# Optimization experiments

Measured on AMD Instinct MI355X. Metric: run time of the kernel, lower is better.

The kernel has to match this reference:

```python
import jax, jax.numpy as jnp
import numpy as np

B, HS, WS = 4, 64, 64
UP = 8
H, W = HS * UP, WS * UP
C_ORI, C_MNT, C_OFF = 90, 180, 8
K = 1024            # max minutiae candidates per image (64*64 cells max 4096)
THRESH = 0.5
DIST_T = 16.0
ANG_T = np.pi / 6


def setup_inputs() -> dict:
    key = jax.random.key(0)
    ks = jax.random.split(key, 8)
    return {
        'segmentation': jax.random.uniform(ks[0], (B, 1, HS, WS), jnp.float32),
        'segmentation_up': jax.random.uniform(ks[1], (B, 1, H, W), jnp.float32),
        'orientation_up': jax.random.normal(ks[2], (B, C_ORI, H, W), jnp.float32),
        'enhanced_real': jax.random.normal(ks[3], (B, 1, H, W), jnp.float32),
        'minutiae_score': jax.random.uniform(ks[4], (B, 1, HS, WS), jnp.float32),
        'minutiae_orientation': jax.random.normal(ks[5], (B, C_MNT, HS, WS), jnp.float32),
        'minutiae_x_offset': jax.random.normal(ks[6], (B, C_OFF, HS, WS), jnp.float32),
        'minutiae_y_offset': jax.random.normal(ks[7], (B, C_OFF, HS, WS), jnp.float32),
    }


def _opening(x, k):
    # morphological opening (erosion then dilation) with a k x k ones kernel,
    # separable min/max pooling; geodesic border (pad so border is neutral).
    pl, pr = (k - 1) // 2, k // 2

    def pool(v, comp, init, pad_val):
        vp = jnp.pad(v, ((0, 0), (pl, pr), (pl, pr)), constant_values=pad_val)
        vp = jax.lax.reduce_window(vp, init, comp, (1, k, 1), (1, 1, 1), 'VALID')
        return jax.lax.reduce_window(vp, init, comp, (1, 1, k), (1, 1, 1), 'VALID')

    er = pool(x, jax.lax.min, np.inf, 1e4)
    return pool(er, jax.lax.max, -np.inf, -1e4)


def _nms_keep(xy, ang, valid):
    # xy: [K,2], ang: [K], valid: [K] bool; entries already sorted by score desc
    d = jnp.sqrt(jnp.sum((xy[:, None, :] - xy[None, :, :]) ** 2, axis=-1))
    da = jnp.abs(ang[:, None] - ang[None, :])
    da = jnp.minimum(da, 2 * jnp.pi - da)
    sup = (d < DIST_T) & (da < ANG_T) & valid[:, None] & valid[None, :]
    idxs = jnp.arange(K)

    def body(i, keep):
        return keep & ~(sup[i] & (idxs > i) & keep[i])

    return jax.lax.fori_loop(0, K, body, valid)


def _detect(score, ori, xo, yo):
    # score: [HS,WS]; ori: [C_MNT,HS,WS]; xo/yo: [C_OFF,HS,WS]
    h, w = score.shape
    flat = score.reshape(-1)
    masked = jnp.where(flat > THRESH, flat, -1.0)
    vals, idx = jax.lax.top_k(masked, K)          # sorted descending
    valid = vals > THRESH
    rows = idx // w
    cols = idx % w
    ang_idx = jnp.argmax(ori.reshape(C_MNT, -1)[:, idx], axis=0)
    xoff = jnp.argmax(xo.reshape(C_OFF, -1)[:, idx], axis=0)
    yoff = jnp.argmax(yo.reshape(C_OFF, -1)[:, idx], axis=0)
    angles = (ang_idx.astype(jnp.float32) * 2.0 - 89.0) * (np.pi / 180.0)
    xc = cols.astype(jnp.float32) * 8.0 + xoff.astype(jnp.float32)
    yc = rows.astype(jnp.float32) * 8.0 + yoff.astype(jnp.float32)
    scores = flat[idx]
    m = jnp.stack([xc, yc, angles, scores], axis=-1)  # [K,4]
    keep = _nms_keep(m[:, :2], angles, valid)
    return m, keep


def reference(segmentation, segmentation_up, orientation_up, enhanced_real,
              minutiae_score, minutiae_orientation, minutiae_x_offset,
              minutiae_y_offset):
    mask = _opening(jnp.round(segmentation[:, 0]), 5)          # [B,HS,WS]
    mask_up = _opening(jnp.round(segmentation_up[:, 0]), 5 * UP)  # [B,H,W]

    score = minutiae_score[:, 0] * mask
    minut, keep = jax.vmap(_detect)(score, minutiae_orientation,
                                    minutiae_x_offset, minutiae_y_offset)
    minut = minut * keep[..., None].astype(minut.dtype)       # zero suppressed

    ori_field = (jnp.argmax(orientation_up, axis=1).astype(jnp.float32) * 2.0
                 - 90.0) * (np.pi / 180.0) * mask_up

    enh = enhanced_real[:, 0] * mask_up
    ef = enh.reshape(B, -1)
    emin = ef.min(axis=1, keepdims=True)
    emax = ef.max(axis=1, keepdims=True)
    enh_vis = ((ef - emin) / (emax - emin + 1e-8)).reshape(B, H, W) * 255.0

    return (minut, keep.astype(jnp.float32), enh_vis, mask_up * 255.0, ori_field)
```

## Files before the change

kernel.cpp:

```cpp
#include <hip/hip_runtime.h>
#include <math.h>

#define HSd 64
#define WSd 64
#define Hh 512
#define Wh 512
#define Bn 4
#define C_ORIc 90
#define C_MNTc 180
#define C_OFFc 8
#define Kc 1024

#define O_MINUT 0
#define O_KEEP  (Bn*Kc*4)
#define O_VIS   (O_KEEP + Bn*Kc)
#define O_MASK  (O_VIS + Bn*Hh*Wh)
#define O_ORI   (O_MASK + Bn*Hh*Wh)

#define PI_180 0.017453292519943295f
#define TWO_PI 6.283185307179586f
#define ANG_T  0.5235987755982988f

template <bool ISMIN, bool BIN>
__global__ __launch_bounds__(256) void pass_v(const float* __restrict__ in,
                                              float* __restrict__ out)
{
    int c = blockIdx.x * 64 + threadIdx.x;
    int r = blockIdx.y * 4 + threadIdx.y;
    int b = blockIdx.z;
    const float* p = in + (size_t)b * Hh * Wh;
    int lo = max(r - 19, 0), hi = min(r + 20, Hh - 1);
    float acc = ISMIN ? 1e30f : -1e30f;
    for (int rr = lo; rr <= hi; rr++) {
        float v = p[rr * Wh + c];
        if (BIN) v = rintf(v);
        acc = ISMIN ? fminf(acc, v) : fmaxf(acc, v);
    }
    out[(size_t)b * Hh * Wh + (size_t)r * Wh + c] = acc;
}

template <bool ISMIN>
__global__ __launch_bounds__(256) void pass_h(const float* __restrict__ in,
                                              float* __restrict__ out)
{
    int c = blockIdx.x * 64 + threadIdx.x;
    int r = blockIdx.y * 4 + threadIdx.y;
    int b = blockIdx.z;
    const float* p = in + (size_t)b * Hh * Wh + (size_t)r * Wh;
    int lo = max(c - 19, 0), hi = min(c + 20, Wh - 1);
    float acc = ISMIN ? 1e30f : -1e30f;
    for (int cc = lo; cc <= hi; cc++)
        acc = ISMIN ? fminf(acc, p[cc]) : fmaxf(acc, p[cc]);
    out[(size_t)b * Hh * Wh + (size_t)r * Wh + c] = acc;
}

__global__ __launch_bounds__(512) void final_up_kernel(const float* __restrict__ vmx,
                                                       const float* __restrict__ ori,
                                                       const float* __restrict__ enh,
                                                       float* __restrict__ out,
                                                       float* __restrict__ partials)
{
    int r = blockIdx.x, b = blockIdx.y, c = threadIdx.x;
    __shared__ float row[512];
    __shared__ float rmn[512];
    __shared__ float rmx[512];
    size_t base = (size_t)b * Hh * Wh + (size_t)r * Wh;
    row[c] = vmx[base + c];
    __syncthreads();
    int lo = max(c - 19, 0), hi = min(c + 20, Wh - 1);
    float m = -1e30f;
    for (int cc = lo; cc <= hi; cc++) m = fmaxf(m, row[cc]);
    out[O_MASK + base + c] = m * 255.0f;

    float of = 0.0f;
    if (m != 0.0f) {
        const float* op = ori + (size_t)b * C_ORIc * Hh * Wh + (size_t)r * Wh + c;
        float best = op[0];
        int bi = 0;
        for (int ch = 1; ch < C_ORIc; ch++) {
            float v = op[(size_t)ch * Hh * Wh];
            if (v > best) { best = v; bi = ch; }
        }
        of = ((float)bi * 2.0f - 90.0f) * PI_180 * m;
    }
    out[O_ORI + base + c] = of;

    float e = enh[base + c] * m;
    rmn[c] = e; rmx[c] = e;
    __syncthreads();
    for (int s2 = 256; s2 > 0; s2 >>= 1) {
        if (c < s2) {
            rmn[c] = fminf(rmn[c], rmn[c + s2]);
            rmx[c] = fmaxf(rmx[c], rmx[c + s2]);
        }
        __syncthreads();
    }
    if (c == 0) {
        partials[(b * Hh + r) * 2 + 0] = rmn[0];
        partials[(b * Hh + r) * 2 + 1] = rmx[0];
    }
}

__global__ __launch_bounds__(512) void reduce_mm_kernel(const float* __restrict__ partials,
                                                        float* __restrict__ mm)
{
    int b = blockIdx.x, t = threadIdx.x;
    __shared__ float mn[512];
    __shared__ float mx[512];
    mn[t] = partials[(b * 512 + t) * 2 + 0];
    mx[t] = partials[(b * 512 + t) * 2 + 1];
    __syncthreads();
    for (int s = 256; s > 0; s >>= 1) {
        if (t < s) {
            mn[t] = fminf(mn[t], mn[t + s]);
            mx[t] = fmaxf(mx[t], mx[t + s]);
        }
        __syncthreads();
    }
    if (t == 0) { mm[b * 2] = mn[0]; mm[b * 2 + 1] = mx[0]; }
}

__global__ __launch_bounds__(256) void vis_kernel(const float* __restrict__ enh,
                                                  const float* __restrict__ maskout,
                                                  const float* __restrict__ mm,
                                                  float* __restrict__ vis)
{
    int idx = blockIdx.x * 256 + threadIdx.x;
    int b = idx >> 18;
    float m = (maskout[idx] != 0.0f) ? 1.0f : 0.0f;
    float e = enh[idx] * m;
    float emin = mm[b * 2], emax = mm[b * 2 + 1];
    float r = (e - emin) / (emax - emin + 1e-8f);
    vis[idx] = r * 255.0f;
}

__global__ __launch_bounds__(1024) void detect_kernel(const float* __restrict__ mscore,
                                                      const float* __restrict__ seg,
                                                      const float* __restrict__ mo,
                                                      const float* __restrict__ xo,
                                                      const float* __restrict__ yo,
                                                      float* __restrict__ out)
{
    int b = blockIdx.x;
    int tid = threadIdx.x;
    __shared__ unsigned long long keys[4096];
    __shared__ float maskT[64][65];
    float* scratch = (float*)keys;

    const float* sg = seg + b * 4096;
    for (int i = tid; i < 4096; i += 1024)
        maskT[i >> 6][i & 63] = rintf(sg[i]);
    __syncthreads();
    for (int i = tid; i < 4096; i += 1024) {
        int r = i >> 6, c = i & 63;
        int lo = max(r - 2, 0), hi = min(r + 2, 63);
        float m = 1e30f;
        for (int rr = lo; rr <= hi; rr++) m = fminf(m, maskT[rr][c]);
        scratch[r * 65 + c] = m;
    }
    __syncthreads();
    for (int i = tid; i < 4096; i += 1024) {
        int r = i >> 6, c = i & 63;
        int lo = max(c - 2, 0), hi = min(c + 2, 63);
        float m = 1e30f;
        for (int cc = lo; cc <= hi; cc++) m = fminf(m, scratch[r * 65 + cc]);
        maskT[r][c] = m;
    }
    __syncthreads();
    for (int i = tid; i < 4096; i += 1024) {
        int r = i >> 6, c = i & 63;
        int lo = max(r - 2, 0), hi = min(r + 2, 63);
        float m = -1e30f;
        for (int rr = lo; rr <= hi; rr++) m = fmaxf(m, maskT[rr][c]);
        scratch[r * 65 + c] = m;
    }
    __syncthreads();
    for (int i = tid; i < 4096; i += 1024) {
        int r = i >> 6, c = i & 63;
        int lo = max(c - 2, 0), hi = min(c + 2, 63);
        float m = -1e30f;
        for (int cc = lo; cc <= hi; cc++) m = fmaxf(m, scratch[r * 65 + cc]);
        maskT[r][c] = m;
    }
    __syncthreads();

    const float* sp = mscore + b * 4096;
    bool anyv = false;
    for (int i = tid; i < 4096; i += 1024) {
        float s = sp[i] * maskT[i >> 6][i & 63];
        anyv |= (s > 0.5f);
    }
    if (!__syncthreads_or(anyv)) {
        float* mout = out + O_MINUT + (size_t)b * Kc * 4 + (size_t)tid * 4;
        mout[0] = 0.f; mout[1] = 0.f; mout[2] = 0.f; mout[3] = 0.f;
        out[O_KEEP + b * Kc + tid] = 0.f;
        return;
    }

    for (int i = tid; i < 4096; i += 1024) {
        float s = sp[i] * maskT[i >> 6][i & 63];
        float mval = (s > 0.5f) ? s : -1.0f;
        unsigned int fb = __float_as_uint(mval);
        unsigned int od = (fb & 0x80000000u) ? ~fb : (fb | 0x80000000u);
        keys[i] = ((unsigned long long)(~od) << 32) | (unsigned int)i;
    }
    for (int k = 2; k <= 4096; k <<= 1) {
        for (int j = k >> 1; j > 0; j >>= 1) {
            __syncthreads();
            for (int t = tid; t < 4096; t += 1024) {
                int ixj = t ^ j;
                if (ixj > t) {
                    unsigned long long va = keys[t], vb = keys[ixj];
                    bool up = ((t & k) == 0);
                    if ((va > vb) == up) { keys[t] = vb; keys[ixj] = va; }
                }
            }
        }
    }
    __syncthreads();

    int idx = (int)(keys[tid] & 0xffffffffu);
    float s = sp[idx] * maskT[idx >> 6][idx & 63];
    bool valid = s > 0.5f;
    int Nv = __syncthreads_count(valid);

    float* sx = scratch;
    float* sy = scratch + 1024;
    float* sa = scratch + 2048;
    int*   keep = (int*)(scratch + 3072);

    float xc = 0.f, yc = 0.f, ang = 0.f;
    if (tid < Nv) {
        int rr = idx >> 6, cc = idx & 63;
        const float* op = mo + (size_t)b * C_MNTc * 4096 + idx;
        float best = op[0]; int bi = 0;
        for (int ch = 1; ch < C_MNTc; ch++) {
            float v = op[ch * 4096];
            if (v > best) { best = v; bi = ch; }
        }
        const float* xp = xo + (size_t)b * C_OFFc * 4096 + idx;
        float bxv = xp[0]; int bx = 0;
        for (int ch = 1; ch < C_OFFc; ch++) {
            float v = xp[ch * 4096];
            if (v > bxv) { bxv = v; bx = ch; }
        }
        const float* yp = yo + (size_t)b * C_OFFc * 4096 + idx;
        float byv = yp[0]; int by = 0;
        for (int ch = 1; ch < C_OFFc; ch++) {
            float v = yp[ch * 4096];
            if (v > byv) { byv = v; by = ch; }
        }
        ang = ((float)bi * 2.0f - 89.0f) * PI_180;
        xc = (float)cc * 8.0f + (float)bx;
        yc = (float)rr * 8.0f + (float)by;
        sx[tid] = xc; sy[tid] = yc; sa[tid] = ang;
        keep[tid] = 1;
    } else {
        keep[tid] = 0;
    }
    __syncthreads();

    for (int i = 0; i < Nv; i++) {
        if (keep[i] && tid > i && tid < Nv && keep[tid]) {
            float dx = sx[tid] - sx[i], dy = sy[tid] - sy[i];
            float d = sqrtf(dx * dx + dy * dy);
            float da = fabsf(sa[tid] - sa[i]);
            da = fminf(da, TWO_PI - da);
            if (d < 16.0f && da < ANG_T) keep[tid] = 0;
        }
        __syncthreads();
    }

    int kf = keep[tid];
    float* mout = out + O_MINUT + (size_t)b * Kc * 4 + (size_t)tid * 4;
    if (kf) {
        mout[0] = xc; mout[1] = yc; mout[2] = ang; mout[3] = s;
    } else {
        mout[0] = 0.f; mout[1] = 0.f; mout[2] = 0.f; mout[3] = 0.f;
    }
    out[O_KEEP + b * Kc + tid] = (float)kf;
}

extern "C" void kernel_launch(void* const* d_in, const int* in_sizes, int n_in,
                              void* d_out_, int out_size, void* d_ws, size_t ws_size,
                              hipStream_t stream)
{
    const float* seg    = (const float*)d_in[0];
    const float* segup  = (const float*)d_in[1];
    const float* oriup  = (const float*)d_in[2];
    const float* enh    = (const float*)d_in[3];
    const float* mscore = (const float*)d_in[4];
    const float* mori   = (const float*)d_in[5];
    const float* mxo    = (const float*)d_in[6];
    const float* myo    = (const float*)d_in[7];
    float* out = (float*)d_out_;

    float* partials = (float*)d_ws;
    float* mm       = partials + Bn * 512 * 2;

    float* T1 = out + O_VIS;
    float* T2 = out + O_ORI;

    detect_kernel<<<Bn, 1024, 0, stream>>>(mscore, seg, mori, mxo, myo, out);

    dim3 pb(64, 4);
    dim3 pg(8, 128, Bn);
    pass_v<true, true><<<pg, pb, 0, stream>>>(segup, T1);
    pass_h<true><<<pg, pb, 0, stream>>>(T1, T2);
    pass_v<false, false><<<pg, pb, 0, stream>>>(T2, T1);
    final_up_kernel<<<dim3(Hh, Bn), 512, 0, stream>>>(T1, oriup, enh, out, partials);
    reduce_mm_kernel<<<Bn, 512, 0, stream>>>(partials, mm);
    vis_kernel<<<(Bn * Hh * Wh) / 256, 256, 0, stream>>>(enh, out + O_MASK, mm, out + O_VIS);
}
```

Before: 511.8 us.

## Fuse detect with vertical erosion and register-block morphology passes

Detection now runs inside the first vertical erosion launch as extra blocks, so the two overlap instead of running as a separate serial kernel. The morphology passes give each thread 4 outputs that share a 37-tap core window, cutting redundant loads, and use float4 IO. The separate min/max reduce kernel is replaced by atomicMin/atomicMax on order-preserving encoded floats, and the detect mask becomes a bitmask. Detection now uses 256 threads with 4 slots each, which may lengthen the serial sort and NMS loops.

```diff
diff --git a/kernel.cpp b/kernel.cpp
--- a/kernel.cpp
+++ b/kernel.cpp
@@ -1,8 +1,6 @@
 #include <hip/hip_runtime.h>
 #include <math.h>
 
-#define HSd 64
-#define WSd 64
 #define Hh 512
 #define Wh 512
 #define Bn 4
@@ -21,264 +19,375 @@
 #define TWO_PI 6.283185307179586f
 #define ANG_T  0.5235987755982988f
 
+#define IMG    262144
+#define PB     (256*Bn)
+
+__device__ __forceinline__ unsigned enc_f(float f) {
+    unsigned u = __float_as_uint(f);
+    return (u & 0x80000000u) ? ~u : (u | 0x80000000u);
+}
+__device__ __forceinline__ float dec_f(unsigned e) {
+    return __uint_as_float((e & 0x80000000u) ? (e ^ 0x80000000u) : ~e);
+}
+
 template <bool ISMIN, bool BIN>
-__global__ __launch_bounds__(256) void pass_v(const float* __restrict__ in,
-                                              float* __restrict__ out)
-{
-    int c = blockIdx.x * 64 + threadIdx.x;
-    int r = blockIdx.y * 4 + threadIdx.y;
-    int b = blockIdx.z;
-    const float* p = in + (size_t)b * Hh * Wh;
-    int lo = max(r - 19, 0), hi = min(r + 20, Hh - 1);
-    float acc = ISMIN ? 1e30f : -1e30f;
-    for (int rr = lo; rr <= hi; rr++) {
-        float v = p[rr * Wh + c];
-        if (BIN) v = rintf(v);
-        acc = ISMIN ? fminf(acc, v) : fmaxf(acc, v);
-    }
-    out[(size_t)b * Hh * Wh + (size_t)r * Wh + c] = acc;
-}
-
-template <bool ISMIN>
-__global__ __launch_bounds__(256) void pass_h(const float* __restrict__ in,
-                                              float* __restrict__ out)
-{
-    int c = blockIdx.x * 64 + threadIdx.x;
-    int r = blockIdx.y * 4 + threadIdx.y;
-    int b = blockIdx.z;
-    const float* p = in + (size_t)b * Hh * Wh + (size_t)r * Wh;
-    int lo = max(c - 19, 0), hi = min(c + 20, Wh - 1);
-    float acc = ISMIN ? 1e30f : -1e30f;
-    for (int cc = lo; cc <= hi; cc++)
-        acc = ISMIN ? fminf(acc, p[cc]) : fmaxf(acc, p[cc]);
-    out[(size_t)b * Hh * Wh + (size_t)r * Wh + c] = acc;
-}
-
-__global__ __launch_bounds__(512) void final_up_kernel(const float* __restrict__ vmx,
-                                                       const float* __restrict__ ori,
-                                                       const float* __restrict__ enh,
-                                                       float* __restrict__ out,
-                                                       float* __restrict__ partials)
-{
-    int r = blockIdx.x, b = blockIdx.y, c = threadIdx.x;
-    __shared__ float row[512];
-    __shared__ float rmn[512];
-    __shared__ float rmx[512];
-    size_t base = (size_t)b * Hh * Wh + (size_t)r * Wh;
-    row[c] = vmx[base + c];
-    __syncthreads();
-    int lo = max(c - 19, 0), hi = min(c + 20, Wh - 1);
-    float m = -1e30f;
-    for (int cc = lo; cc <= hi; cc++) m = fmaxf(m, row[cc]);
-    out[O_MASK + base + c] = m * 255.0f;
-
-    float of = 0.0f;
-    if (m != 0.0f) {
-        const float* op = ori + (size_t)b * C_ORIc * Hh * Wh + (size_t)r * Wh + c;
-        float best = op[0];
-        int bi = 0;
-        for (int ch = 1; ch < C_ORIc; ch++) {
-            float v = op[(size_t)ch * Hh * Wh];
-            if (v > best) { best = v; bi = ch; }
-        }
-        of = ((float)bi * 2.0f - 90.0f) * PI_180 * m;
-    }
-    out[O_ORI + base + c] = of;
-
-    float e = enh[base + c] * m;
-    rmn[c] = e; rmx[c] = e;
-    __syncthreads();
-    for (int s2 = 256; s2 > 0; s2 >>= 1) {
-        if (c < s2) {
-            rmn[c] = fminf(rmn[c], rmn[c + s2]);
-            rmx[c] = fmaxf(rmx[c], rmx[c + s2]);
-        }
-        __syncthreads();
-    }
-    if (c == 0) {
-        partials[(b * Hh + r) * 2 + 0] = rmn[0];
-        partials[(b * Hh + r) * 2 + 1] = rmx[0];
-    }
-}
-
-__global__ __launch_bounds__(512) void reduce_mm_kernel(const float* __restrict__ partials,
-                                                        float* __restrict__ mm)
-{
-    int b = blockIdx.x, t = threadIdx.x;
-    __shared__ float mn[512];
-    __shared__ float mx[512];
-    mn[t] = partials[(b * 512 + t) * 2 + 0];
-    mx[t] = partials[(b * 512 + t) * 2 + 1];
-    __syncthreads();
-    for (int s = 256; s > 0; s >>= 1) {
-        if (t < s) {
-            mn[t] = fminf(mn[t], mn[t + s]);
-            mx[t] = fmaxf(mx[t], mx[t + s]);
-        }
-        __syncthreads();
-    }
-    if (t == 0) { mm[b * 2] = mn[0]; mm[b * 2 + 1] = mx[0]; }
-}
-
-__global__ __launch_bounds__(256) void vis_kernel(const float* __restrict__ enh,
-                                                  const float* __restrict__ maskout,
-                                                  const float* __restrict__ mm,
-                                                  float* __restrict__ vis)
-{
-    int idx = blockIdx.x * 256 + threadIdx.x;
-    int b = idx >> 18;
-    float m = (maskout[idx] != 0.0f) ? 1.0f : 0.0f;
-    float e = enh[idx] * m;
-    float emin = mm[b * 2], emax = mm[b * 2 + 1];
-    float r = (e - emin) / (emax - emin + 1e-8f);
-    vis[idx] = r * 255.0f;
-}
-
-__global__ __launch_bounds__(1024) void detect_kernel(const float* __restrict__ mscore,
-                                                      const float* __restrict__ seg,
-                                                      const float* __restrict__ mo,
-                                                      const float* __restrict__ xo,
-                                                      const float* __restrict__ yo,
-                                                      float* __restrict__ out)
-{
-    int b = blockIdx.x;
+__device__ __forceinline__ void vert_pass_body(const float* __restrict__ in,
+                                               float* __restrict__ outp, int blk)
+{
+    const float SENT = ISMIN ? 1e30f : -1e30f;
+    int b  = blk >> 8;
+    int rg = (blk >> 3) & 31;
+    int cg = blk & 7;
+    int tx = threadIdx.x & 63, ty = threadIdx.x >> 6;
+    int c  = cg * 64 + tx;
+    int r0 = rg * 16 + ty * 4;
+    const float* p = in + (size_t)b * IMG + c;
+
+    #define LDV(rr) (((rr) >= 0 && (rr) < 512) ? (BIN ? rintf(p[(rr) * 512]) \
+                                                      : p[(rr) * 512]) : SENT)
+    #define OPV(a, bb) (ISMIN ? fminf(a, bb) : fmaxf(a, bb))
+    float core = SENT;
+    #pragma unroll
+    for (int k = 0; k < 37; k++) core = OPV(core, LDV(r0 - 16 + k));
+    float L2v = LDV(r0 - 17);
+    float L1v = OPV(LDV(r0 - 18), L2v);
+    float L0v = OPV(LDV(r0 - 19), L1v);
+    float H1v = LDV(r0 + 21);
+    float H2v = OPV(H1v, LDV(r0 + 22));
+    float H3v = OPV(H2v, LDV(r0 + 23));
+    float* q = outp + (size_t)b * IMG + (size_t)r0 * 512 + c;
+    q[0]    = OPV(core, L0v);
+    q[512]  = OPV(core, OPV(L1v, H1v));
+    q[1024] = OPV(core, OPV(L2v, H2v));
+    q[1536] = OPV(core, H3v);
+    #undef LDV
+    #undef OPV
+}
+
+__global__ __launch_bounds__(256) void k1_vert_erode_detect(
+    const float* __restrict__ segup, const float* __restrict__ mscore,
+    const float* __restrict__ seg, const float* __restrict__ mo,
+    const float* __restrict__ xo, const float* __restrict__ yo,
+    float* __restrict__ out, float* __restrict__ T1, unsigned* __restrict__ mmu)
+{
+    __shared__ union {
+        unsigned long long keys[4096];
+        float scr[8320];
+    } U;
+    __shared__ unsigned smBits[128];
+    __shared__ unsigned short smHalf[256];
+
     int tid = threadIdx.x;
-    __shared__ unsigned long long keys[4096];
-    __shared__ float maskT[64][65];
-    float* scratch = (float*)keys;
+    if (blockIdx.x < PB) {
+        vert_pass_body<true, true>(segup, T1, blockIdx.x);
+        return;
+    }
+
+    int b = blockIdx.x - PB;
+    if (tid == 0) { mmu[b * 2] = 0xFFFFFFFFu; mmu[b * 2 + 1] = 0u; }
 
     const float* sg = seg + b * 4096;
-    for (int i = tid; i < 4096; i += 1024)
-        maskT[i >> 6][i & 63] = rintf(sg[i]);
-    __syncthreads();
-    for (int i = tid; i < 4096; i += 1024) {
+    float* scr0 = U.scr;
+    float* scr1 = U.scr + 4160;
+    for (int i = tid; i < 4096; i += 256)
+        scr0[(i >> 6) * 65 + (i & 63)] = rintf(sg[i]);
+    __syncthreads();
+    for (int i = tid; i < 4096; i += 256) {
         int r = i >> 6, c = i & 63;
         int lo = max(r - 2, 0), hi = min(r + 2, 63);
         float m = 1e30f;
-        for (int rr = lo; rr <= hi; rr++) m = fminf(m, maskT[rr][c]);
-        scratch[r * 65 + c] = m;
-    }
-    __syncthreads();
-    for (int i = tid; i < 4096; i += 1024) {
+        for (int rr = lo; rr <= hi; rr++) m = fminf(m, scr0[rr * 65 + c]);
+        scr1[r * 65 + c] = m;
+    }
+    __syncthreads();
+    for (int i = tid; i < 4096; i += 256) {
         int r = i >> 6, c = i & 63;
         int lo = max(c - 2, 0), hi = min(c + 2, 63);
         float m = 1e30f;
-        for (int cc = lo; cc <= hi; cc++) m = fminf(m, scratch[r * 65 + cc]);
-        maskT[r][c] = m;
-    }
-    __syncthreads();
-    for (int i = tid; i < 4096; i += 1024) {
+        for (int cc = lo; cc <= hi; cc++) m = fminf(m, scr1[r * 65 + cc]);
+        scr0[r * 65 + c] = m;
+    }
+    __syncthreads();
+    for (int i = tid; i < 4096; i += 256) {
         int r = i >> 6, c = i & 63;
         int lo = max(r - 2, 0), hi = min(r + 2, 63);
         float m = -1e30f;
-        for (int rr = lo; rr <= hi; rr++) m = fmaxf(m, maskT[rr][c]);
-        scratch[r * 65 + c] = m;
-    }
-    __syncthreads();
-    for (int i = tid; i < 4096; i += 1024) {
-        int r = i >> 6, c = i & 63;
-        int lo = max(c - 2, 0), hi = min(c + 2, 63);
-        float m = -1e30f;
-        for (int cc = lo; cc <= hi; cc++) m = fmaxf(m, scratch[r * 65 + cc]);
-        maskT[r][c] = m;
-    }
+        for (int rr = lo; rr <= hi; rr++) m = fmaxf(m, scr0[rr * 65 + c]);
+        scr1[r * 65 + c] = m;
+    }
+    __syncthreads();
+    {
+        unsigned short bits16 = 0;
+        int i0 = tid * 16;
+        int r = i0 >> 6;
+        for (int j = 0; j < 16; j++) {
+            int c = (i0 + j) & 63;
+            int lo = max(c - 2, 0), hi = min(c + 2, 63);
+            float m = -1e30f;
+            for (int cc = lo; cc <= hi; cc++) m = fmaxf(m, scr1[r * 65 + cc]);
+            bits16 |= ((unsigned short)(m != 0.0f)) << j;
+        }
+        smHalf[tid] = bits16;
+    }
+    __syncthreads();
+    if (tid < 128)
+        smBits[tid] = (unsigned)smHalf[2 * tid] | ((unsigned)smHalf[2 * tid + 1] << 16);
     __syncthreads();
 
     const float* sp = mscore + b * 4096;
     bool anyv = false;
-    for (int i = tid; i < 4096; i += 1024) {
-        float s = sp[i] * maskT[i >> 6][i & 63];
-        anyv |= (s > 0.5f);
+    for (int i = tid; i < 4096; i += 256) {
+        unsigned m = (smBits[i >> 5] >> (i & 31)) & 1u;
+        anyv |= (m && sp[i] > 0.5f);
     }
     if (!__syncthreads_or(anyv)) {
-        float* mout = out + O_MINUT + (size_t)b * Kc * 4 + (size_t)tid * 4;
-        mout[0] = 0.f; mout[1] = 0.f; mout[2] = 0.f; mout[3] = 0.f;
-        out[O_KEEP + b * Kc + tid] = 0.f;
+        float4 z = {0.f, 0.f, 0.f, 0.f};
+        float4* mo4 = (float4*)(out + O_MINUT + (size_t)b * 4096);
+        for (int i = tid; i < 1024; i += 256) mo4[i] = z;
+        ((float4*)(out + O_KEEP + (size_t)b * 1024))[tid] = z;
         return;
     }
 
-    for (int i = tid; i < 4096; i += 1024) {
-        float s = sp[i] * maskT[i >> 6][i & 63];
+    for (int i = tid; i < 4096; i += 256) {
+        unsigned m = (smBits[i >> 5] >> (i & 31)) & 1u;
+        float s = m ? sp[i] : 0.0f;
         float mval = (s > 0.5f) ? s : -1.0f;
-        unsigned int fb = __float_as_uint(mval);
-        unsigned int od = (fb & 0x80000000u) ? ~fb : (fb | 0x80000000u);
-        keys[i] = ((unsigned long long)(~od) << 32) | (unsigned int)i;
+        unsigned fb = __float_as_uint(mval);
+        unsigned od = (fb & 0x80000000u) ? ~fb : (fb | 0x80000000u);
+        U.keys[i] = ((unsigned long long)(~od) << 32) | (unsigned)i;
     }
     for (int k = 2; k <= 4096; k <<= 1) {
         for (int j = k >> 1; j > 0; j >>= 1) {
             __syncthreads();
-            for (int t = tid; t < 4096; t += 1024) {
+            for (int t = tid; t < 4096; t += 256) {
                 int ixj = t ^ j;
                 if (ixj > t) {
-                    unsigned long long va = keys[t], vb = keys[ixj];
+                    unsigned long long va = U.keys[t], vb = U.keys[ixj];
                     bool up = ((t & k) == 0);
-                    if ((va > vb) == up) { keys[t] = vb; keys[ixj] = va; }
+                    if ((va > vb) == up) { U.keys[t] = vb; U.keys[ixj] = va; }
                 }
             }
         }
     }
     __syncthreads();
 
-    int idx = (int)(keys[tid] & 0xffffffffu);
-    float s = sp[idx] * maskT[idx >> 6][idx & 63];
-    bool valid = s > 0.5f;
-    int Nv = __syncthreads_count(valid);
-
-    float* sx = scratch;
-    float* sy = scratch + 1024;
-    float* sa = scratch + 2048;
-    int*   keep = (int*)(scratch + 3072);
-
-    float xc = 0.f, yc = 0.f, ang = 0.f;
-    if (tid < Nv) {
-        int rr = idx >> 6, cc = idx & 63;
-        const float* op = mo + (size_t)b * C_MNTc * 4096 + idx;
-        float best = op[0]; int bi = 0;
-        for (int ch = 1; ch < C_MNTc; ch++) {
-            float v = op[ch * 4096];
-            if (v > best) { best = v; bi = ch; }
-        }
-        const float* xp = xo + (size_t)b * C_OFFc * 4096 + idx;
-        float bxv = xp[0]; int bx = 0;
-        for (int ch = 1; ch < C_OFFc; ch++) {
-            float v = xp[ch * 4096];
-            if (v > bxv) { bxv = v; bx = ch; }
-        }
-        const float* yp = yo + (size_t)b * C_OFFc * 4096 + idx;
-        float byv = yp[0]; int by = 0;
-        for (int ch = 1; ch < C_OFFc; ch++) {
-            float v = yp[ch * 4096];
-            if (v > byv) { byv = v; by = ch; }
-        }
-        ang = ((float)bi * 2.0f - 89.0f) * PI_180;
-        xc = (float)cc * 8.0f + (float)bx;
-        yc = (float)rr * 8.0f + (float)by;
-        sx[tid] = xc; sy[tid] = yc; sa[tid] = ang;
-        keep[tid] = 1;
-    } else {
-        keep[tid] = 0;
+    int idxs[4]; float ss[4]; int vld[4];
+    int Nv = 0;
+    for (int j = 0; j < 4; j++) {
+        int slot = tid + j * 256;
+        int idx = (int)(U.keys[slot] & 0xffffffffu);
+        unsigned m = (smBits[idx >> 5] >> (idx & 31)) & 1u;
+        float s = m ? sp[idx] : 0.0f;
+        idxs[j] = idx; ss[j] = s; vld[j] = (s > 0.5f);
+        Nv += __syncthreads_count(vld[j]);
+    }
+
+    float xcs[4], ycs[4], angs[4];
+    for (int j = 0; j < 4; j++) {
+        int slot = tid + j * 256;
+        xcs[j] = ycs[j] = angs[j] = 0.f;
+        if (slot < Nv) {
+            int idx = idxs[j];
+            int rr = idx >> 6, cc = idx & 63;
+            const float* op_ = mo + (size_t)b * C_MNTc * 4096 + idx;
+            float best = op_[0]; int bi = 0;
+            for (int ch = 1; ch < C_MNTc; ch++) {
+                float v = op_[ch * 4096];
+                if (v > best) { best = v; bi = ch; }
+            }
+            const float* xp = xo + (size_t)b * C_OFFc * 4096 + idx;
+            float bxv = xp[0]; int bx = 0;
+            for (int ch = 1; ch < C_OFFc; ch++) {
+                float v = xp[ch * 4096];
+                if (v > bxv) { bxv = v; bx = ch; }
+            }
+            const float* yp = yo + (size_t)b * C_OFFc * 4096 + idx;
+            float byv = yp[0]; int by = 0;
+            for (int ch = 1; ch < C_OFFc; ch++) {
+                float v = yp[ch * 4096];
+                if (v > byv) { byv = v; by = ch; }
+            }
+            angs[j] = ((float)bi * 2.0f - 89.0f) * PI_180;
+            xcs[j]  = (float)cc * 8.0f + (float)bx;
+            ycs[j]  = (float)rr * 8.0f + (float)by;
+        }
+    }
+    __syncthreads();
+    float* sx = U.scr;
+    float* sy = U.scr + 1024;
+    float* sa = U.scr + 2048;
+    int*   keep = (int*)(U.scr + 3072);
+    for (int j = 0; j < 4; j++) {
+        int slot = tid + j * 256;
+        sx[slot] = xcs[j]; sy[slot] = ycs[j]; sa[slot] = angs[j];
+        keep[slot] = (slot < Nv) ? 1 : 0;
     }
     __syncthreads();
 
     for (int i = 0; i < Nv; i++) {
-        if (keep[i] && tid > i && tid < Nv && keep[tid]) {
-            float dx = sx[tid] - sx[i], dy = sy[tid] - sy[i];
-            float d = sqrtf(dx * dx + dy * dy);
-            float da = fabsf(sa[tid] - sa[i]);
-            da = fminf(da, TWO_PI - da);
-            if (d < 16.0f && da < ANG_T) keep[tid] = 0;
+        if (keep[i]) {
+            float xi = sx[i], yi = sy[i], ai = sa[i];
+            for (int j = 0; j < 4; j++) {
+                int slot = tid + j * 256;
+                if (slot > i && slot < Nv && keep[slot]) {
+                    float dx = xcs[j] - xi, dy = ycs[j] - yi;
+                    float d = sqrtf(dx * dx + dy * dy);
+                    float da = fabsf(angs[j] - ai);
+                    da = fminf(da, TWO_PI - da);
+                    if (d < 16.0f && da < ANG_T) keep[slot] = 0;
+                }
+            }
         }
         __syncthreads();
     }
-
-    int kf = keep[tid];
-    float* mout = out + O_MINUT + (size_t)b * Kc * 4 + (size_t)tid * 4;
-    if (kf) {
-        mout[0] = xc; mout[1] = yc; mout[2] = ang; mout[3] = s;
-    } else {
-        mout[0] = 0.f; mout[1] = 0.f; mout[2] = 0.f; mout[3] = 0.f;
-    }
-    out[O_KEEP + b * Kc + tid] = (float)kf;
+    for (int j = 0; j < 4; j++) {
+        int slot = tid + j * 256;
+        int kf = keep[slot];
+        float* mout = out + O_MINUT + (size_t)b * 4096 + slot * 4;
+        if (kf) {
+            mout[0] = xcs[j]; mout[1] = ycs[j]; mout[2] = angs[j]; mout[3] = ss[j];
+        } else {
+            mout[0] = 0.f; mout[1] = 0.f; mout[2] = 0.f; mout[3] = 0.f;
+        }
+        out[O_KEEP + b * 1024 + slot] = (float)kf;
+    }
+}
+
+__global__ __launch_bounds__(512) void k2_horiz_erode(const float* __restrict__ T1,
+                                                      float* __restrict__ T2)
+{
+    __shared__ float row[4][512];
+    int b = blockIdx.y;
+    int r0 = blockIdx.x * 4;
+    int tx = threadIdx.x, ty = threadIdx.y;
+    const float* p = T1 + (size_t)b * IMG + (size_t)(r0 + ty) * 512;
+    ((float4*)row[ty])[tx] = ((const float4*)p)[tx];
+    __syncthreads();
+    int c0 = tx * 4;
+    const float* rw = row[ty];
+    #define LDH(cc) (((cc) >= 0 && (cc) < 512) ? rw[cc] : 1e30f)
+    float core = 1e30f;
+    #pragma unroll
+    for (int k = 0; k < 37; k++) core = fminf(core, LDH(c0 - 16 + k));
+    float L2v = LDH(c0 - 17);
+    float L1v = fminf(LDH(c0 - 18), L2v);
+    float L0v = fminf(LDH(c0 - 19), L1v);
+    float H1v = LDH(c0 + 21);
+    float H2v = fminf(H1v, LDH(c0 + 22));
+    float H3v = fminf(H2v, LDH(c0 + 23));
+    #undef LDH
+    float4 o;
+    o.x = fminf(core, L0v);
+    o.y = fminf(core, fminf(L1v, H1v));
+    o.z = fminf(core, fminf(L2v, H2v));
+    o.w = fminf(core, H3v);
+    ((float4*)(T2 + (size_t)b * IMG + (size_t)(r0 + ty) * 512))[tx] = o;
+}
+
+__global__ __launch_bounds__(256) void k3_vert_dilate(const float* __restrict__ T2,
+                                                      float* __restrict__ T3)
+{
+    vert_pass_body<false, false>(T2, T3, blockIdx.x);
+}
+
+__global__ __launch_bounds__(512) void k4_final(const float* __restrict__ T3,
+                                                const float* __restrict__ ori,
+                                                const float* __restrict__ enh,
+                                                float* __restrict__ out,
+                                                unsigned* __restrict__ mmu)
+{
+    __shared__ float row[4][512];
+    __shared__ float red[512];
+    int b = blockIdx.y;
+    int r0 = blockIdx.x * 4;
+    int tx = threadIdx.x, ty = threadIdx.y;
+    int ltid = ty * 128 + tx;
+    const float* p = T3 + (size_t)b * IMG + (size_t)(r0 + ty) * 512;
+    ((float4*)row[ty])[tx] = ((const float4*)p)[tx];
+    __syncthreads();
+    int c0 = tx * 4;
+    const float* rw = row[ty];
+    #define LDD(cc) (((cc) >= 0 && (cc) < 512) ? rw[cc] : -1e30f)
+    float core = -1e30f;
+    #pragma unroll
+    for (int k = 0; k < 37; k++) core = fmaxf(core, LDD(c0 - 16 + k));
+    float L2v = LDD(c0 - 17);
+    float L1v = fmaxf(LDD(c0 - 18), L2v);
+    float L0v = fmaxf(LDD(c0 - 19), L1v);
+    float H1v = LDD(c0 + 21);
+    float H2v = fmaxf(H1v, LDD(c0 + 22));
+    float H3v = fmaxf(H2v, LDD(c0 + 23));
+    #undef LDD
+    float m[4];
+    m[0] = fmaxf(core, L0v);
+    m[1] = fmaxf(core, fmaxf(L1v, H1v));
+    m[2] = fmaxf(core, fmaxf(L2v, H2v));
+    m[3] = fmaxf(core, H3v);
+
+    size_t base = (size_t)b * IMG + (size_t)(r0 + ty) * 512 + c0;
+    float4 mk = {m[0] * 255.f, m[1] * 255.f, m[2] * 255.f, m[3] * 255.f};
+    *((float4*)(out + O_MASK + base)) = mk;
+
+    float ov[4];
+    for (int j = 0; j < 4; j++) {
+        ov[j] = 0.0f;
+        if (m[j] != 0.0f) {
+            const float* op_ = ori + (size_t)b * C_ORIc * IMG
+                             + (size_t)(r0 + ty) * 512 + (c0 + j);
+            float best = op_[0];
+            int bi = 0;
+            for (int ch = 1; ch < C_ORIc; ch++) {
+                float v = op_[(size_t)ch * IMG];
+                if (v > best) { best = v; bi = ch; }
+            }
+            ov[j] = ((float)bi * 2.0f - 90.0f) * PI_180 * m[j];
+        }
+    }
+    float4 o4 = {ov[0], ov[1], ov[2], ov[3]};
+    *((float4*)(out + O_ORI + base)) = o4;
+
+    float4 e4 = ((const float4*)(enh + (size_t)b * IMG + (size_t)(r0 + ty) * 512))[tx];
+    float e0 = e4.x * m[0], e1 = e4.y * m[1], e2 = e4.z * m[2], e3 = e4.w * m[3];
+    float lmin = fminf(fminf(e0, e1), fminf(e2, e3));
+    float lmax = fmaxf(fmaxf(e0, e1), fmaxf(e2, e3));
+
+    red[ltid] = lmin;
+    __syncthreads();
+    for (int s = 256; s > 0; s >>= 1) {
+        if (ltid < s) red[ltid] = fminf(red[ltid], red[ltid + s]);
+        __syncthreads();
+    }
+    float bmin = red[0];
+    __syncthreads();
+    red[ltid] = lmax;
+    __syncthreads();
+    for (int s = 256; s > 0; s >>= 1) {
+        if (ltid < s) red[ltid] = fmaxf(red[ltid], red[ltid + s]);
+        __syncthreads();
+    }
+    if (ltid == 0) {
+        atomicMin(&mmu[b * 2 + 0], enc_f(bmin));
+        atomicMax(&mmu[b * 2 + 1], enc_f(red[0]));
+    }
+}
+
+__global__ __launch_bounds__(256) void k5_vis(const float* __restrict__ enh,
+                                              const float* __restrict__ maskout,
+                                              const unsigned* __restrict__ mmu,
+                                              float* __restrict__ vis)
+{
+    int i4 = blockIdx.x * 256 + threadIdx.x;
+    int b = i4 >> 16;
+    float4 e = ((const float4*)enh)[i4];
+    float4 mk = ((const float4*)maskout)[i4];
+    float emin = dec_f(mmu[b * 2]);
+    float den = dec_f(mmu[b * 2 + 1]) - emin + 1e-8f;
+    float4 o;
+    o.x = (e.x * (mk.x != 0.f ? 1.f : 0.f) - emin) / den * 255.0f;
+    o.y = (e.y * (mk.y != 0.f ? 1.f : 0.f) - emin) / den * 255.0f;
+    o.z = (e.z * (mk.z != 0.f ? 1.f : 0.f) - emin) / den * 255.0f;
+    o.w = (e.w * (mk.w != 0.f ? 1.f : 0.f) - emin) / den * 255.0f;
+    ((float4*)vis)[i4] = o;
 }
 
 extern "C" void kernel_launch(void* const* d_in, const int* in_sizes, int n_in,
@@ -295,20 +404,16 @@
     const float* myo    = (const float*)d_in[7];
     float* out = (float*)d_out_;
 
-    float* partials = (float*)d_ws;
-    float* mm       = partials + Bn * 512 * 2;
-
-    float* T1 = out + O_VIS;
-    float* T2 = out + O_ORI;
-
-    detect_kernel<<<Bn, 1024, 0, stream>>>(mscore, seg, mori, mxo, myo, out);
-
-    dim3 pb(64, 4);
-    dim3 pg(8, 128, Bn);
-    pass_v<true, true><<<pg, pb, 0, stream>>>(segup, T1);
-    pass_h<true><<<pg, pb, 0, stream>>>(T1, T2);
-    pass_v<false, false><<<pg, pb, 0, stream>>>(T2, T1);
-    final_up_kernel<<<dim3(Hh, Bn), 512, 0, stream>>>(T1, oriup, enh, out, partials);
-    reduce_mm_kernel<<<Bn, 512, 0, stream>>>(partials, mm);
-    vis_kernel<<<(Bn * Hh * Wh) / 256, 256, 0, stream>>>(enh, out + O_MASK, mm, out + O_VIS);
-}
+    unsigned* mmu = (unsigned*)d_ws;
+    float* T1 = (float*)d_ws + 16;
+    float* T2 = T1 + Bn * IMG;
+    float* T3 = T2 + Bn * IMG;
+
+    k1_vert_erode_detect<<<PB + Bn, 256, 0, stream>>>(segup, mscore, seg, mori,
+                                                      mxo, myo, out, T1, mmu);
+    k2_horiz_erode<<<dim3(128, Bn), dim3(128, 4), 0, stream>>>(T1, T2);
+    k3_vert_dilate<<<PB, 256, 0, stream>>>(T2, T3);
+    k4_final<<<dim3(128, Bn), dim3(128, 4), 0, stream>>>(T3, oriup, enh, out, mmu);
+    k5_vis<<<(Bn * IMG) / 1024, 256, 0, stream>>>(enh, out + O_MASK, mmu,
+                                                  out + O_VIS);
+}
```

Result: faster. 483.7 us (-5.5%).
